# Kernel tuning notes

Hardware: AMD Instinct MI355X
Metric: run time of the kernel (lower is better)

The kernel has to match this reference:

```python
import jax, jax.numpy as jnp
import numpy as np
import math

IN_FEATURES = 4096
OUT_FEATURES = 4096
P = max(IN_FEATURES, OUT_FEATURES)   # total_permutations
D = min(IN_FEATURES, OUT_FEATURES)   # diag_length
SPARSITY = 0.1
K = math.ceil(int((1.0 - SPARSITY) * IN_FEATURES * OUT_FEATURES) / D)  # 3687
ALPHA_LR = 0.01
NUM_ITER = 50


def sparse_soft_topk_mask_dykstra(alpha, k, l, num_iter):
    """Dykstra projection of alpha/l onto {0<=m<=1, sum(m)=k} (soft top-k mask)."""
    s = alpha / l
    n = s.shape[0]
    p0 = jnp.zeros_like(s)
    q0 = jnp.zeros_like(s)

    def body(carry, _):
        x, p, q = carry
        # project x+p onto hyperplane sum = k
        t = x + p
        y = t + (k - jnp.sum(t)) / n
        p = t - y
        # project y+q onto box [0, 1]
        u = y + q
        x_new = jnp.clip(u, 0.0, 1.0)
        q = u - x_new
        return (x_new, p, q), None

    (x, _, _), _ = jax.lax.scan(body, (s, p0, q0), None, length=num_iter)
    return x  # last projection is onto the box -> exact zeros / ones


def compute_weight(V, alpha):
    a = sparse_soft_topk_mask_dykstra(alpha, K, ALPHA_LR, NUM_ITER)  # (P,)
    vals = a[:, None] * V                                             # (P, D)
    i = jnp.arange(P)[:, None]
    j = jnp.arange(D)[None, :]
    if OUT_FEATURES >= IN_FEATURES:
        # pseudo-diagonal i: rows shifted by i, column j scaled by V[i, j]
        rows = (i + j) % OUT_FEATURES
        cols = jnp.broadcast_to(j, (P, D))
    else:
        # row r scaled by V[i, r], columns shifted by i
        rows = jnp.broadcast_to(j, (P, D))
        cols = (i + j) % IN_FEATURES
    W = jnp.zeros((OUT_FEATURES, IN_FEATURES), V.dtype)
    W = W.at[rows.reshape(-1), cols.reshape(-1)].add(vals.reshape(-1))
    return W


def setup_inputs() -> dict:
    key = jax.random.key(0)
    k1, k2 = jax.random.split(key)
    # kaiming_uniform_(a=sqrt(5)) over fan_in = D -> bound = sqrt(1/D)
    bound = 1.0 / np.sqrt(D)
    V = jax.random.uniform(k1, (P, D), jnp.float32, -bound, bound)
    alpha = jnp.ones((P,), jnp.float32) / IN_FEATURES
    x = jax.random.normal(k2, (512, IN_FEATURES), jnp.float32)
    return {"x": x, "V": V, "alpha": alpha}


def reference(x, V, alpha):
    W = compute_weight(V, alpha)  # (out, in)
    return x @ W.T                # F.linear(x, W)
```

## Files before the change

### kernel.cpp

```cpp
#include <hip/hip_runtime.h>
#include <hip/hip_bf16.h>
#include <stdint.h>

#define PDIM 4096
#define KSEL 3687.0f
#define NITER 50

typedef unsigned short ushort_t;
typedef __attribute__((ext_vector_type(8))) __bf16 bf16x8;
typedef __attribute__((ext_vector_type(4))) float f32x4;

typedef __attribute__((address_space(3))) void lds_void;
typedef __attribute__((address_space(1))) const void glob_void;

__device__ __forceinline__ ushort_t f32_to_bf16_rne(float f) {
  union { float f; uint32_t u; } v; v.f = f;
  uint32_t r = 0x7FFFu + ((v.u >> 16) & 1u);
  return (ushort_t)((v.u + r) >> 16);
}

__device__ __forceinline__ float bf16_to_f32(ushort_t h) {
  union { uint32_t u; float f; } v; v.u = ((uint32_t)h) << 16;
  return v.f;
}

__device__ __forceinline__ void async_cp16(const void* g, void* l) {
  __builtin_amdgcn_global_load_lds((glob_void*)g, (lds_void*)l, 16, 0, 0);
}

__device__ __forceinline__ void raw_barrier() {
  __builtin_amdgcn_sched_barrier(0);
  asm volatile("" ::: "memory");
  __builtin_amdgcn_s_barrier();
  asm volatile("" ::: "memory");
  __builtin_amdgcn_sched_barrier(0);
}

__device__ __forceinline__ float wave_sum_dpp(float x) {
  float s = x;
  int t;
  t = __builtin_amdgcn_update_dpp(0, __float_as_int(s), 0x111, 0xF, 0xF, true);
  s += __int_as_float(t);
  t = __builtin_amdgcn_update_dpp(0, __float_as_int(s), 0x112, 0xF, 0xF, true);
  s += __int_as_float(t);
  t = __builtin_amdgcn_update_dpp(0, __float_as_int(s), 0x114, 0xF, 0xF, true);
  s += __int_as_float(t);
  t = __builtin_amdgcn_update_dpp(0, __float_as_int(s), 0x118, 0xF, 0xF, true);
  s += __int_as_float(t);
  t = __builtin_amdgcn_update_dpp(0, __float_as_int(s), 0x142, 0xA, 0xF, true);
  s += __int_as_float(t);
  t = __builtin_amdgcn_update_dpp(0, __float_as_int(s), 0x143, 0xC, 0xF, true);
  s += __int_as_float(t);
  return s;
}

__global__ __launch_bounds__(256) void prep_kernel(
    const float* __restrict__ alpha, float* __restrict__ a_out,
    const float* __restrict__ x, ushort_t* __restrict__ Xb, int n4,
    const float* __restrict__ V) {
  if (blockIdx.x >= 1 && blockIdx.x <= 2048) {
    const float4* V4 = (const float4*)V;
    const int base = (blockIdx.x - 1) * 2048 + (int)threadIdx.x;
#pragma unroll
    for (int i = 0; i < 8; ++i) {
      const float4 vv = V4[base + i * 256];
      asm volatile("" :: "v"(vv.x), "v"(vv.y), "v"(vv.z), "v"(vv.w));
    }
    return;
  }
  if (blockIdx.x != 0) {
    const int i = (blockIdx.x - 2049) * 256 + threadIdx.x;
    if (i < n4) {
      const float4 v = ((const float4*)x)[i];
      ushort4 o;
      o.x = f32_to_bf16_rne(v.x);
      o.y = f32_to_bf16_rne(v.y);
      o.z = f32_to_bf16_rne(v.z);
      o.w = f32_to_bf16_rne(v.w);
      ((ushort4*)Xb)[i] = o;
    }
    return;
  }
  __shared__ float red[8];
  const int tid = threadIdx.x;
  const int lane = tid & 63;
  const int wv = tid >> 6;
  float xx[16], q[16];
  float p = 0.0f;
#pragma unroll
  for (int i = 0; i < 16; ++i) {
    xx[i] = alpha[i * 256 + tid] * 100.0f;
    q[i] = 0.0f;
  }
  for (int it = 0; it < NITER; ++it) {
    float t[16];
    float loc = 0.0f;
#pragma unroll
    for (int i = 0; i < 16; ++i) { t[i] = xx[i] + p; loc += t[i]; }
    loc = wave_sum_dpp(loc);
    const int slot = (it & 1) * 4;
    if (lane == 63) red[slot + wv] = loc;
    __syncthreads();
    const float tot = red[slot] + red[slot + 1] + red[slot + 2] + red[slot + 3];
    const float corr = (KSEL - tot) * (1.0f / 4096.0f);
    p = -corr;
#pragma unroll
    for (int i = 0; i < 16; ++i) {
      const float y = t[i] + corr;
      const float u = y + q[i];
      const float xn = fminf(fmaxf(u, 0.0f), 1.0f);
      q[i] = u - xn;
      xx[i] = xn;
    }
  }
#pragma unroll
  for (int i = 0; i < 16; ++i) a_out[i * 256 + tid] = xx[i];
}

__global__ __launch_bounds__(256) void wmat_kernel(
    const float* __restrict__ V, const float* __restrict__ a,
    ushort_t* __restrict__ Wb) {
  __shared__ float vt[192][67];
  const int t = threadIdx.x;
  const int r0 = blockIdx.x * 128;
  const int c0 = blockIdx.y * 64;
  const int dbase = (r0 - c0 - 63 + 2 * PDIM) & (PDIM - 1);
  const int csub = (t & 15) * 4;
  const int rsub = t >> 4;
#pragma unroll
  for (int i = 0; i < 12; ++i) {
    const int ld = i * 16 + rsub;
    const int d = (dbase + ld) & (PDIM - 1);
    const float av = a[d];
    const float4 vv = *(const float4*)(V + (size_t)d * PDIM + c0 + csub);
    vt[ld][csub + 0] = av * vv.x;
    vt[ld][csub + 1] = av * vv.y;
    vt[ld][csub + 2] = av * vv.z;
    vt[ld][csub + 3] = av * vv.w;
  }
  __syncthreads();
#pragma unroll
  for (int k = 0; k < 4; ++k) {
    const int ry = (t >> 3) + k * 32;
    const int cb = (t & 7) * 8;
    ushort_t pk[8];
#pragma unroll
    for (int j = 0; j < 8; ++j) {
      const int c = cb + j;
      pk[j] = f32_to_bf16_rne(vt[ry - c + 63][c]);
    }
    *(uint4*)(Wb + (size_t)(r0 + ry) * PDIM + c0 + cb) = *(const uint4*)pk;
  }
}

__global__ __launch_bounds__(512, 2) void gemm_kernel(
    const ushort_t* __restrict__ Xb, const ushort_t* __restrict__ Wb,
    ushort_t* __restrict__ par) {
  constexpr int Kdim = 4096, KQ = 512, NIT = KQ / 64;
  __shared__ __align__(16) ushort_t As[2][256 * 64];
  __shared__ __align__(16) ushort_t Bs[2][256 * 64];
  const int tid = threadIdx.x;
  const int lane = tid & 63;
  const int w = tid >> 6;
  const int l15 = lane & 15;
  const int quad = lane >> 4;
  const int wr = w >> 2;
  const int wc = w & 3;
  const int bid = blockIdx.x;
  const int z = bid & 7;
  const int tile = bid >> 3;
  const int mblk = tile & 1;
  const int nblk = tile >> 1;
  const int m0 = mblk * 256;
  const int n0 = nblk * 256;
  const int kbase = z * KQ;
  const int crow8 = lane >> 3;
  const int slotj = lane & 7;

  f32x4 acc[8][4];
#pragma unroll
  for (int mt = 0; mt < 8; ++mt)
#pragma unroll
    for (int nt = 0; nt < 4; ++nt) acc[mt][nt] = (f32x4){0.f, 0.f, 0.f, 0.f};

  auto stage = [&](int buf, int it) {
    const int k0 = kbase + it * 64;
#pragma unroll
    for (int i = 0; i < 4; ++i) {
      const int chunk = w * 4 + i;
      const int row = chunk * 8 + crow8;
      const int j = slotj ^ (row & 7);
      async_cp16(Xb + (size_t)(m0 + row) * Kdim + k0 + j * 8,
                 (char*)&As[buf][0] + (size_t)chunk * 1024);
      async_cp16(Wb + (size_t)(n0 + row) * Kdim + k0 + j * 8,
                 (char*)&Bs[buf][0] + (size_t)chunk * 1024);
    }
  };

  stage(0, 0);
  for (int it = 0; it < NIT; ++it) {
    const int cur = it & 1;
    if (it < NIT - 1) {
      stage(cur ^ 1, it + 1);
      asm volatile("s_waitcnt vmcnt(8)" ::: "memory");
    } else {
      asm volatile("s_waitcnt vmcnt(0)" ::: "memory");
    }
    raw_barrier();
    const ushort_t* __restrict__ Ab = &As[cur][0];
    const ushort_t* __restrict__ Bb = &Bs[cur][0];
    bf16x8 bfr[4][2];
#pragma unroll
    for (int nt = 0; nt < 4; ++nt)
#pragma unroll
      for (int k2 = 0; k2 < 2; ++k2) {
        const int row = wc * 64 + nt * 16 + l15;
        const int cj = k2 * 4 + quad;
        bfr[nt][k2] = *(const bf16x8*)&Bb[(row * 8 + (cj ^ (row & 7))) * 8];
      }
#pragma unroll
    for (int mh = 0; mh < 2; ++mh) {
      bf16x8 afr[4][2];
#pragma unroll
      for (int mi = 0; mi < 4; ++mi)
#pragma unroll
        for (int k2 = 0; k2 < 2; ++k2) {
          const int row = wr * 128 + (mh * 4 + mi) * 16 + l15;
          const int cj = k2 * 4 + quad;
          afr[mi][k2] = *(const bf16x8*)&Ab[(row * 8 + (cj ^ (row & 7))) * 8];
        }
#pragma unroll
      for (int mi = 0; mi < 4; ++mi)
#pragma unroll
        for (int nt = 0; nt < 4; ++nt) {
          acc[mh * 4 + mi][nt] = __builtin_amdgcn_mfma_f32_16x16x32_bf16(
              afr[mi][0], bfr[nt][0], acc[mh * 4 + mi][nt], 0, 0, 0);
          acc[mh * 4 + mi][nt] = __builtin_amdgcn_mfma_f32_16x16x32_bf16(
              afr[mi][1], bfr[nt][1], acc[mh * 4 + mi][nt], 0, 0, 0);
        }
    }
    raw_barrier();
  }
  ushort_t* pbase = par + ((size_t)z * 32 + tile) * 65536;
#pragma unroll
  for (int mt = 0; mt < 8; ++mt) {
#pragma unroll
    for (int nt = 0; nt < 4; ++nt) {
      const int slot = mt * 4 + nt;
      ushort4 o;
      o.x = f32_to_bf16_rne(acc[mt][nt][0]);
      o.y = f32_to_bf16_rne(acc[mt][nt][1]);
      o.z = f32_to_bf16_rne(acc[mt][nt][2]);
      o.w = f32_to_bf16_rne(acc[mt][nt][3]);
      *(ushort4*)(pbase + (size_t)(slot * 512 + tid) * 4) = o;
    }
  }
}

__global__ __launch_bounds__(512) void combine_kernel(
    const ushort_t* __restrict__ par, float* __restrict__ out) {
  const int tile = blockIdx.x >> 2;
  const int qh = blockIdx.x & 3;
  const int mblk = tile & 1;
  const int nblk = tile >> 1;
  const int m0 = mblk * 256;
  const int n0 = nblk * 256;
  const int tid = threadIdx.x;
  const int lane = tid & 63;
  const int w = tid >> 6;
  const int wr = w >> 2;
  const int wc = w & 3;
  const int l15 = lane & 15;
  const int quad = lane >> 4;
#pragma unroll
  for (int ss = 0; ss < 8; ++ss) {
    const int slot = qh * 8 + ss;
    float s0 = 0.f, s1 = 0.f, s2 = 0.f, s3 = 0.f;
#pragma unroll
    for (int z = 0; z < 8; ++z) {
      const ushort4 v = *(const ushort4*)(par +
          ((size_t)z * 32 + tile) * 65536 + (size_t)(slot * 512 + tid) * 4);
      s0 += bf16_to_f32(v.x);
      s1 += bf16_to_f32(v.y);
      s2 += bf16_to_f32(v.z);
      s3 += bf16_to_f32(v.w);
    }
    const int mt = slot >> 2;
    const int nt = slot & 3;
    const int mb = m0 + wr * 128 + mt * 16 + quad * 4;
    const int n = n0 + wc * 64 + nt * 16 + l15;
    out[(size_t)(mb + 0) * PDIM + n] = s0;
    out[(size_t)(mb + 1) * PDIM + n] = s1;
    out[(size_t)(mb + 2) * PDIM + n] = s2;
    out[(size_t)(mb + 3) * PDIM + n] = s3;
  }
}

extern "C" void kernel_launch(void* const* d_in, const int* in_sizes, int n_in,
                              void* d_out, int out_size, void* d_ws,
                              size_t ws_size, hipStream_t stream) {
  const float* x = (const float*)d_in[0];
  const float* V = (const float*)d_in[1];
  const float* alpha = (const float*)d_in[2];
  float* out = (float*)d_out;
  const int M = in_sizes[0] / PDIM;

  float* a_mask = (float*)d_ws;
  ushort_t* Xb = (ushort_t*)((char*)d_ws + 16 * 1024);
  ushort_t* Wb = Xb + (size_t)M * PDIM;
  ushort_t* par = Wb + (size_t)PDIM * PDIM;

  const int n4x = (M * PDIM) / 4;
  prep_kernel<<<1 + 2048 + (n4x + 255) / 256, 256, 0, stream>>>(
      alpha, a_mask, x, Xb, n4x, V);
  wmat_kernel<<<dim3(PDIM / 128, PDIM / 64), 256, 0, stream>>>(V, a_mask, Wb);
  gemm_kernel<<<256, 512, 0, stream>>>(Xb, Wb, par);
  combine_kernel<<<128, 512, 0, stream>>>(par, out);
}
```

Measured before the change: 152.7 us.

## Interleave GEMM prefetch with MFMA in quarter phases and remap block order

The split-K GEMM main loop is restructured into four phases per K-step. Each phase issues a quarter of the next tile's async global-to-LDS copies, loads a slice of A fragments, and runs the matching MFMAs at raised priority, with barriers between phases. This aims to overlap memory traffic with matrix math more finely than the previous double-buffered loop. The block index is also remapped so consecutive blocks take different tiles of the same K-split rather than different K-splits of the same tile, which changes L2 reuse. The change adds more barriers per iteration and a full vmcnt wait each step, which could cost more than the finer overlap gains.

New measurement: 155.8 us. No clear change (+2.0%).

```diff
diff --git a/kernel.cpp b/kernel.cpp
--- a/kernel.cpp
+++ b/kernel.cpp
@@ -167,8 +167,9 @@
   const int wr = w >> 2;
   const int wc = w & 3;
   const int bid = blockIdx.x;
-  const int z = bid & 7;
-  const int tile = bid >> 3;
+  const int u = (bid & 7) * 32 + (bid >> 3);
+  const int z = u & 7;
+  const int tile = u >> 3;
   const int mblk = tile & 1;
   const int nblk = tile >> 1;
   const int m0 = mblk * 256;
@@ -183,63 +184,73 @@
 #pragma unroll
     for (int nt = 0; nt < 4; ++nt) acc[mt][nt] = (f32x4){0.f, 0.f, 0.f, 0.f};
 
-  auto stage = [&](int buf, int it) {
+  auto stage_half = [&](int buf, int it, int q) {
     const int k0 = kbase + it * 64;
-#pragma unroll
-    for (int i = 0; i < 4; ++i) {
-      const int chunk = w * 4 + i;
+    const int half = q & 1;
+#pragma unroll
+    for (int L = 0; L < 2; ++L) {
+      const int chunk = half * 16 + L * 8 + w;
       const int row = chunk * 8 + crow8;
       const int j = slotj ^ (row & 7);
-      async_cp16(Xb + (size_t)(m0 + row) * Kdim + k0 + j * 8,
-                 (char*)&As[buf][0] + (size_t)chunk * 1024);
-      async_cp16(Wb + (size_t)(n0 + row) * Kdim + k0 + j * 8,
-                 (char*)&Bs[buf][0] + (size_t)chunk * 1024);
+      if (q < 2)
+        async_cp16(Xb + (size_t)(m0 + row) * Kdim + k0 + j * 8,
+                   (char*)&As[buf][0] + (size_t)chunk * 1024);
+      else
+        async_cp16(Wb + (size_t)(n0 + row) * Kdim + k0 + j * 8,
+                   (char*)&Bs[buf][0] + (size_t)chunk * 1024);
     }
   };
 
-  stage(0, 0);
-  for (int it = 0; it < NIT; ++it) {
-    const int cur = it & 1;
-    if (it < NIT - 1) {
-      stage(cur ^ 1, it + 1);
-      asm volatile("s_waitcnt vmcnt(8)" ::: "memory");
-    } else {
-      asm volatile("s_waitcnt vmcnt(0)" ::: "memory");
-    }
-    raw_barrier();
+#pragma unroll
+  for (int q = 0; q < 4; ++q) stage_half(0, 0, q);
+  asm volatile("s_waitcnt vmcnt(0)" ::: "memory");
+  raw_barrier();
+
+  for (int t = 0; t < NIT; ++t) {
+    const int cur = t & 1;
     const ushort_t* __restrict__ Ab = &As[cur][0];
     const ushort_t* __restrict__ Bb = &Bs[cur][0];
     bf16x8 bfr[4][2];
 #pragma unroll
-    for (int nt = 0; nt < 4; ++nt)
-#pragma unroll
-      for (int k2 = 0; k2 < 2; ++k2) {
-        const int row = wc * 64 + nt * 16 + l15;
-        const int cj = k2 * 4 + quad;
-        bfr[nt][k2] = *(const bf16x8*)&Bb[(row * 8 + (cj ^ (row & 7))) * 8];
+    for (int q = 0; q < 4; ++q) {
+      if (t + 1 < NIT) stage_half(cur ^ 1, t + 1, q);
+      if (q == 0) {
+#pragma unroll
+        for (int nt = 0; nt < 4; ++nt)
+#pragma unroll
+          for (int k2 = 0; k2 < 2; ++k2) {
+            const int row = wc * 64 + nt * 16 + l15;
+            const int cj = k2 * 4 + quad;
+            bfr[nt][k2] =
+                *(const bf16x8*)&Bb[(row * 8 + (cj ^ (row & 7))) * 8];
+          }
       }
-#pragma unroll
-    for (int mh = 0; mh < 2; ++mh) {
-      bf16x8 afr[4][2];
-#pragma unroll
-      for (int mi = 0; mi < 4; ++mi)
+      bf16x8 afr[2][2];
+#pragma unroll
+      for (int mi = 0; mi < 2; ++mi)
 #pragma unroll
         for (int k2 = 0; k2 < 2; ++k2) {
-          const int row = wr * 128 + (mh * 4 + mi) * 16 + l15;
+          const int row = wr * 128 + (q * 2 + mi) * 16 + l15;
           const int cj = k2 * 4 + quad;
           afr[mi][k2] = *(const bf16x8*)&Ab[(row * 8 + (cj ^ (row & 7))) * 8];
         }
-#pragma unroll
-      for (int mi = 0; mi < 4; ++mi)
+      raw_barrier();
+      asm volatile("s_waitcnt lgkmcnt(0)" ::: "memory");
+      __builtin_amdgcn_sched_barrier(0);
+      __builtin_amdgcn_s_setprio(1);
+#pragma unroll
+      for (int mi = 0; mi < 2; ++mi)
 #pragma unroll
         for (int nt = 0; nt < 4; ++nt) {
-          acc[mh * 4 + mi][nt] = __builtin_amdgcn_mfma_f32_16x16x32_bf16(
-              afr[mi][0], bfr[nt][0], acc[mh * 4 + mi][nt], 0, 0, 0);
-          acc[mh * 4 + mi][nt] = __builtin_amdgcn_mfma_f32_16x16x32_bf16(
-              afr[mi][1], bfr[nt][1], acc[mh * 4 + mi][nt], 0, 0, 0);
+          acc[q * 2 + mi][nt] = __builtin_amdgcn_mfma_f32_16x16x32_bf16(
+              afr[mi][0], bfr[nt][0], acc[q * 2 + mi][nt], 0, 0, 0);
+          acc[q * 2 + mi][nt] = __builtin_amdgcn_mfma_f32_16x16x32_bf16(
+              afr[mi][1], bfr[nt][1], acc[q * 2 + mi][nt], 0, 0, 0);
         }
-    }
-    raw_barrier();
+      __builtin_amdgcn_s_setprio(0);
+      if (q == 3) asm volatile("s_waitcnt vmcnt(0)" ::: "memory");
+      raw_barrier();
+    }
   }
   ushort_t* pbase = par + ((size_t)z * 32 + tile) * 65536;
 #pragma unroll
```
